# Performance work log

Measured on AMD Instinct MI355X. Metric: run time of the kernel, lower is better.

## Reference

```python
import jax, jax.numpy as jnp
import numpy as np

NUM_HEADS = 16
TOP_K = 6


def setup_inputs() -> dict:
    key = jax.random.key(0)
    ks = jax.random.split(key, 16)
    B, P = 8192, 4096
    QD = PD = D = 1024  # query_dim, prototype_dim, token_dim
    s = lambda d: 1.0 / np.sqrt(d)
    return {
        "query": jax.random.normal(ks[0], (B, QD), jnp.float32),
        "prototype_bank": jax.random.normal(ks[1], (P, PD), jnp.float32),
        "prototype_logits": jax.random.normal(ks[2], (B, P), jnp.float32),
        # query_proj / prototype_proj (torch Linear: y = x @ W.T + b)
        "Wq_proj": jax.random.normal(ks[3], (D, QD), jnp.float32) * s(QD),
        "bq_proj": jnp.zeros((D,), jnp.float32),
        "Wp_proj": jax.random.normal(ks[4], (D, PD), jnp.float32) * s(PD),
        "bp_proj": jnp.zeros((D,), jnp.float32),
        # MultiheadAttention in-proj (q, k, v) and out-proj
        "Wq": jax.random.normal(ks[5], (D, D), jnp.float32) * s(D),
        "bq": jnp.zeros((D,), jnp.float32),
        "Wk": jax.random.normal(ks[6], (D, D), jnp.float32) * s(D),
        "bk": jnp.zeros((D,), jnp.float32),
        "Wv": jax.random.normal(ks[7], (D, D), jnp.float32) * s(D),
        "bv": jnp.zeros((D,), jnp.float32),
        "Wo": jax.random.normal(ks[8], (D, D), jnp.float32) * s(D),
        "bo": jnp.zeros((D,), jnp.float32),
    }


def reference(query, prototype_bank, prototype_logits,
              Wq_proj, bq_proj, Wp_proj, bp_proj,
              Wq, bq, Wk, bk, Wv, bv, Wo, bo):
    B, D = query.shape[0], Wq.shape[0]
    h = NUM_HEADS
    dh = D // h
    k = min(TOP_K, prototype_bank.shape[0])

    # top-k prototype selection (indices only)
    _, topk_idx = jax.lax.top_k(prototype_logits, k)            # [B, k]

    projected_bank = prototype_bank @ Wp_proj.T + bp_proj        # [P, D]
    selected = projected_bank[topk_idx]                          # [B, k, D]

    attn_query = (query @ Wq_proj.T + bq_proj)[:, None, :]       # [B, 1, D]

    # MultiheadAttention (batch_first, eval mode so dropout is a no-op)
    qh = (attn_query @ Wq.T + bq).reshape(B, 1, h, dh).transpose(0, 2, 1, 3)  # [B,h,1,dh]
    kh = (selected @ Wk.T + bk).reshape(B, k, h, dh).transpose(0, 2, 1, 3)    # [B,h,k,dh]
    vh = (selected @ Wv.T + bv).reshape(B, k, h, dh).transpose(0, 2, 1, 3)    # [B,h,k,dh]

    scores = jnp.einsum("bhqd,bhkd->bhqk", qh, kh) / jnp.sqrt(jnp.float32(dh))
    w = jax.nn.softmax(scores, axis=-1)                          # [B,h,1,k]
    ctx = jnp.einsum("bhqk,bhkd->bhqd", w, vh)                   # [B,h,1,dh]
    ctx = ctx.transpose(0, 2, 1, 3).reshape(B, 1, D)
    context = ctx @ Wo.T + bo                                    # [B,1,D]

    attn_weights = w.mean(axis=1)                                # avg heads -> [B,1,k]
    return context[:, 0, :], attn_weights[:, 0, :]
```

## Files before the change

kernel.cpp:

```cpp
#include <hip/hip_runtime.h>
#include <stdint.h>

#define B_ROWS 8192
#define P_ROWS 4096
#define D_DIM  1024
#define K_TOP  6

typedef __attribute__((ext_vector_type(8))) short short8;
typedef __attribute__((ext_vector_type(4))) float floatx4;

static __device__ __forceinline__ float bf2f(unsigned short h) {
  return __uint_as_float(((unsigned)h) << 16);
}
static __device__ __forceinline__ unsigned short f2bf(float f) {
  unsigned u = __float_as_uint(f);
  u += 0x7FFFu + ((u >> 16) & 1u);
  return (unsigned short)(u >> 16);
}

typedef __attribute__((address_space(3))) unsigned int lds32_t;
typedef const __attribute__((address_space(1))) unsigned int g32_t;

static __device__ __forceinline__ void gld_lds16(const unsigned short* g, unsigned short* l) {
  __builtin_amdgcn_global_load_lds((g32_t*)(uintptr_t)g,
                                   (lds32_t*)(unsigned int)(uintptr_t)l, 16, 0, 0);
}

template <bool OUT_BF16, bool HAS_BIAS>
static __device__ __forceinline__ void gemm_bt_body(
    const unsigned short* __restrict__ A, const unsigned short* __restrict__ Bw,
    const float* __restrict__ bias, void* __restrict__ Cout, int m0, int n0) {
  constexpr int Kd = 1024, Nd = 1024, BK = 64;
  __shared__ unsigned short sA[128 * BK];
  __shared__ unsigned short sB[128 * BK];

  const int tid = threadIdx.x;
  const int wid = tid >> 6, lane = tid & 63;
  const int wm = (wid & 1) * 64, wn = (wid >> 1) * 64;

  floatx4 acc[4][4];
#pragma unroll
  for (int mt = 0; mt < 4; ++mt)
#pragma unroll
    for (int nt = 0; nt < 4; ++nt) acc[mt][nt] = (floatx4){0.f, 0.f, 0.f, 0.f};

  const int ld_row = lane >> 3;
  const int ld_col = (lane & 7) * 8;

  for (int kt = 0; kt < Kd / BK; ++kt) {
    const int k0 = kt * BK;
    __syncthreads();
#pragma unroll
    for (int c = 0; c < 4; ++c) {
      const int ch = wid * 4 + c;
      const int r = ch * 8 + ld_row;
      gld_lds16(A  + (size_t)(m0 + r) * Kd + k0 + ld_col, sA + ch * 512);
      gld_lds16(Bw + (size_t)(n0 + r) * Kd + k0 + ld_col, sB + ch * 512);
    }
    __syncthreads();
#pragma unroll
    for (int ks = 0; ks < 2; ++ks) {
      const int kk = ks * 32 + (lane >> 4) * 8;
      short8 a[4], b[4];
#pragma unroll
      for (int t = 0; t < 4; ++t) {
        a[t] = *(const short8*)(sA + (wm + t * 16 + (lane & 15)) * BK + kk);
        b[t] = *(const short8*)(sB + (wn + t * 16 + (lane & 15)) * BK + kk);
      }
#pragma unroll
      for (int mt = 0; mt < 4; ++mt)
#pragma unroll
        for (int nt = 0; nt < 4; ++nt)
          acc[mt][nt] = __builtin_amdgcn_mfma_f32_16x16x32_bf16(a[mt], b[nt], acc[mt][nt], 0, 0, 0);
    }
  }

  const int er = lane >> 4;
  const int ec = lane & 15;
#pragma unroll
  for (int mt = 0; mt < 4; ++mt) {
#pragma unroll
    for (int nt = 0; nt < 4; ++nt) {
      const int col = n0 + wn + nt * 16 + ec;
      const float bv = HAS_BIAS ? bias[col] : 0.f;
#pragma unroll
      for (int r = 0; r < 4; ++r) {
        const int row = m0 + wm + mt * 16 + er * 4 + r;
        const float v = acc[mt][nt][r] + bv;
        if (OUT_BF16)
          ((unsigned short*)Cout)[(size_t)row * Nd + col] = f2bf(v);
        else
          ((float*)Cout)[(size_t)row * Nd + col] = v;
      }
    }
  }
}

template <bool OUT_BF16>
__global__ __launch_bounds__(256) void gemm_bt_kernel(
    const unsigned short* __restrict__ A, const unsigned short* __restrict__ Bw,
    const float* __restrict__ bias, void* __restrict__ Cout) {
  gemm_bt_body<OUT_BF16, true>(A, Bw, bias, Cout, blockIdx.y * 128, blockIdx.x * 128);
}

static __device__ __forceinline__ void cswap64(unsigned long long& hi, unsigned long long& lo) {
  unsigned long long x = hi, y = lo;
  bool c = y > x;
  hi = c ? y : x;
  lo = c ? x : y;
}

static __device__ __forceinline__ unsigned long long topk_key(float val, int idx) {
  unsigned u = __float_as_uint(val);
  u ^= ((unsigned)((int)u >> 31)) | 0x80000000u;
  return (((unsigned long long)u) << 32) | (unsigned long long)(0xFFFFFFFFu - (unsigned)idx);
}

#define PREP_BLOCKS 25856
struct PrepArgs {
  const float* cs[6]; unsigned short* cd[6];
  const float* ts[2]; unsigned short* td[2];
  const float* bW[3]; const float* bp[3]; const float* bb[3]; float* bo[3];
  const float* logits; int* topk;
};

__global__ __launch_bounds__(256) void prep_kernel(PrepArgs a) {
  const int b0 = blockIdx.x;
  if (b0 < 8192) {
    __shared__ float s_tau[4];
    __shared__ int s_cnt;
    __shared__ unsigned long long s_cand[128];
    const int row = b0;
    const int tid = threadIdx.x;
    const int wid = tid >> 6, lane = tid & 63;
    const float4* lp4 = (const float4*)(a.logits + (size_t)row * P_ROWS);

    if (tid == 0) s_cnt = 0;

    float4 r0 = lp4[tid];
    float4 r1 = lp4[256 + tid];
    float4 r2 = lp4[512 + tid];
    float4 r3 = lp4[768 + tid];
    float tmax =
        fmaxf(fmaxf(fmaxf(fmaxf(r0.x, r0.y), fmaxf(r0.z, r0.w)),
                    fmaxf(fmaxf(r1.x, r1.y), fmaxf(r1.z, r1.w))),
              fmaxf(fmaxf(fmaxf(r2.x, r2.y), fmaxf(r2.z, r2.w)),
                    fmaxf(fmaxf(r3.x, r3.y), fmaxf(r3.z, r3.w))));

    float mkeep = tmax, tau = tmax;
#pragma unroll
    for (int it = 0; it < K_TOP; ++it) {
      float best = mkeep;
#pragma unroll
      for (int o = 32; o > 0; o >>= 1) best = fmaxf(best, __shfl_xor(best, o));
      tau = best;
      if (it < K_TOP - 1) mkeep = (mkeep == best) ? -1e38f : mkeep;
    }
    if (lane == 0) s_tau[wid] = tau;
    __syncthreads();
    tau = fmaxf(fmaxf(s_tau[0], s_tau[1]), fmaxf(s_tau[2], s_tau[3]));

    if (tmax >= tau) {
      float4 q0 = lp4[tid];
      float4 q1 = lp4[256 + tid];
      float4 q2 = lp4[512 + tid];
      float4 q3 = lp4[768 + tid];
      auto push = [&](float v, int idx) {
        if (v >= tau) {
          int s = atomicAdd(&s_cnt, 1);
          if (s < 128) s_cand[s] = topk_key(v, idx);
        }
      };
      const int e0 = tid * 4, e1 = 1024 + tid * 4, e2 = 2048 + tid * 4, e3 = 3072 + tid * 4;
      push(q0.x, e0); push(q0.y, e0 + 1); push(q0.z, e0 + 2); push(q0.w, e0 + 3);
      push(q1.x, e1); push(q1.y, e1 + 1); push(q1.z, e1 + 2); push(q1.w, e1 + 3);
      push(q2.x, e2); push(q2.y, e2 + 1); push(q2.z, e2 + 2); push(q2.w, e2 + 3);
      push(q3.x, e3); push(q3.y, e3 + 1); push(q3.z, e3 + 2); push(q3.w, e3 + 3);
    }
    __syncthreads();
    const int n = s_cnt;
    if (wid != 0) return;

    if (n <= 128) {
      unsigned long long k0 = (lane < n) ? s_cand[lane] : 0ull;
      unsigned long long k1 = (lane + 64 < n) ? s_cand[lane + 64] : 0ull;
#pragma unroll
      for (int it = 0; it < K_TOP; ++it) {
        unsigned long long best = k0 > k1 ? k0 : k1;
#pragma unroll
        for (int o = 32; o > 0; o >>= 1) {
          unsigned long long t = __shfl_xor(best, o);
          best = t > best ? t : best;
        }
        if (lane == 0)
          a.topk[row * K_TOP + it] = (int)(0xFFFFFFFFu - (unsigned)(best & 0xFFFFFFFFull));
        k0 = (k0 == best) ? 0ull : k0;
        k1 = (k1 == best) ? 0ull : k1;
      }
    } else {
      unsigned long long m0 = 0, m1 = 0, m2 = 0, m3 = 0, m4 = 0, m5 = 0;
      auto ins = [&](float val, int idx) {
        unsigned long long key = topk_key(val, idx);
        m5 = key > m5 ? key : m5;
        cswap64(m4, m5);
        cswap64(m3, m4);
        cswap64(m2, m3);
        cswap64(m1, m2);
        cswap64(m0, m1);
      };
      for (int j = 0; j < 16; ++j) {
        float4 v = lp4[j * 64 + lane];
        const int base = j * 256 + lane * 4;
        ins(v.x, base);
        ins(v.y, base + 1);
        ins(v.z, base + 2);
        ins(v.w, base + 3);
      }
#pragma unroll
      for (int it = 0; it < K_TOP; ++it) {
        unsigned long long best = m0;
#pragma unroll
        for (int o = 32; o > 0; o >>= 1) {
          unsigned long long t = __shfl_xor(best, o);
          best = t > best ? t : best;
        }
        if (lane == 0)
          a.topk[row * K_TOP + it] = (int)(0xFFFFFFFFu - (unsigned)(best & 0xFFFFFFFFull));
        const bool pred = (m0 == best);
        m0 = pred ? m1 : m0;
        m1 = pred ? m2 : m1;
        m2 = pred ? m3 : m2;
        m3 = pred ? m4 : m3;
        m4 = pred ? m5 : m4;
        m5 = pred ? 0ull : m5;
      }
    }
    return;
  }
  const int b = b0 - 8192;
  if (b < 16384) {
    int seg; unsigned sb;
    if (b < 8192) { seg = 0; sb = 0; }
    else if (b < 12288) { seg = 1; sb = 8192; }
    else { seg = 2 + ((b - 12288) >> 10); sb = 12288u + (((unsigned)(seg - 2)) << 10); }
    const unsigned off = (((unsigned)b - sb) << 10) + threadIdx.x * 4u;
    float4 v = *(const float4*)(a.cs[seg] + off);
    ushort4 o;
    o.x = f2bf(v.x); o.y = f2bf(v.y); o.z = f2bf(v.z); o.w = f2bf(v.w);
    *(ushort4*)(a.cd[seg] + off) = o;
  } else if (b < 16896) {
    __shared__ unsigned short t[64][72];
    const int tt = b - 16384;
    const int which = tt >> 8;
    const int tile = tt & 255;
    const int i0 = (tile >> 4) * 64, j0 = (tile & 15) * 64;
    const float* src = a.ts[which];
    unsigned short* dst = a.td[which];
    const int r = threadIdx.x >> 4;
    const int c = (threadIdx.x & 15) * 4;
#pragma unroll
    for (int rr = 0; rr < 4; ++rr) {
      const int row = r + rr * 16;
      float4 v = *(const float4*)(src + (size_t)(i0 + row) * D_DIM + j0 + c);
      t[c + 0][row] = f2bf(v.x); t[c + 1][row] = f2bf(v.y);
      t[c + 2][row] = f2bf(v.z); t[c + 3][row] = f2bf(v.w);
    }
    __syncthreads();
#pragma unroll
    for (int rr = 0; rr < 4; ++rr) {
      const int row = r + rr * 16;
      ushort4 v = *(const ushort4*)(&t[row][c]);
      *(ushort4*)(dst + (size_t)(j0 + row) * D_DIM + i0 + c) = v;
    }
  } else {
    const int b3 = b - 16896;
    const int j = b3 >> 8;
    const int nb = b3 & 255;
    const int wid = threadIdx.x >> 6, lane = threadIdx.x & 63;
    const int n = nb * 4 + wid;
    const float* W = a.bW[j] + (size_t)n * D_DIM;
    const float* p = a.bp[j];
    float s = 0.f;
#pragma unroll
    for (int d = lane; d < D_DIM; d += 64) s += W[d] * p[d];
#pragma unroll
    for (int o = 32; o > 0; o >>= 1) s += __shfl_xor(s, o);
    if (lane == 0) a.bo[j][n] = s + a.bb[j][n];
  }
}

#define MID_BLOCKS 192
struct MidArgs {
  const unsigned short* fA[3]; const unsigned short* fW[3]; unsigned short* fC[3];
};

__global__ __launch_bounds__(256) void mid_kernel(MidArgs a) {
  const int z = blockIdx.x >> 6;
  const int tile = blockIdx.x & 63;
  gemm_bt_body<true, false>(a.fA[z], a.fW[z], nullptr, (void*)a.fC[z],
                            (tile >> 3) * 128, (tile & 7) * 128);
}

#define GEMM3_BLOCKS 1024
struct Gemm3Args {
  const unsigned short* A[3]; const unsigned short* W[3]; const float* bias[3];
  unsigned short* C[3];
};

__global__ __launch_bounds__(256) void gemm3_kernel(Gemm3Args a) {
  const int b = blockIdx.x;
  int seg, lb;
  if (b < 512) { seg = 0; lb = b; }
  else if (b < 768) { seg = 1; lb = b - 512; }
  else { seg = 2; lb = b - 768; }
  gemm_bt_body<true, true>(a.A[seg], a.W[seg], a.bias[seg], (void*)a.C[seg],
                           (lb >> 3) * 128, (lb & 7) * 128);
}

__global__ __launch_bounds__(256) void attn_kernel(
    const unsigned short* __restrict__ q2,
    const unsigned short* __restrict__ kb,
    const unsigned short* __restrict__ vb,
    const int* __restrict__ topk,
    unsigned short* __restrict__ ctx,
    float* __restrict__ attnw) {
  const int wid = threadIdx.x >> 6, lane = threadIdx.x & 63;
  const int b = blockIdx.x * 4 + wid;

  int idx[K_TOP];
#pragma unroll
  for (int j = 0; j < K_TOP; ++j) idx[j] = topk[b * K_TOP + j];

  const short8* q2r = (const short8*)(q2 + (size_t)b * D_DIM);
  short8 qv0 = q2r[lane], qv1 = q2r[64 + lane];
  float q0[8], q1[8];
#pragma unroll
  for (int i = 0; i < 8; ++i) {
    q0[i] = bf2f((unsigned short)qv0[i]);
    q1[i] = bf2f((unsigned short)qv1[i]);
  }

  float s0[K_TOP], s1[K_TOP];
#pragma unroll
  for (int j = 0; j < K_TOP; ++j) {
    const short8* kr = (const short8*)(kb + (size_t)idx[j] * D_DIM);
    short8 k0 = kr[lane], k1 = kr[64 + lane];
    float p0 = 0.f, p1 = 0.f;
#pragma unroll
    for (int i = 0; i < 8; ++i) {
      p0 += q0[i] * bf2f((unsigned short)k0[i]);
      p1 += q1[i] * bf2f((unsigned short)k1[i]);
    }
    s0[j] = p0; s1[j] = p1;
  }
#pragma unroll
  for (int j = 0; j < K_TOP; ++j) {
#pragma unroll
    for (int o = 1; o < 8; o <<= 1) {
      s0[j] += __shfl_xor(s0[j], o);
      s1[j] += __shfl_xor(s1[j], o);
    }
  }

  float mx0 = -1e30f, mx1 = -1e30f;
#pragma unroll
  for (int j = 0; j < K_TOP; ++j) {
    mx0 = fmaxf(mx0, s0[j] * 0.125f);
    mx1 = fmaxf(mx1, s1[j] * 0.125f);
  }
  float w0[K_TOP], w1[K_TOP], sum0 = 0.f, sum1 = 0.f;
#pragma unroll
  for (int j = 0; j < K_TOP; ++j) {
    w0[j] = __expf(s0[j] * 0.125f - mx0); sum0 += w0[j];
    w1[j] = __expf(s1[j] * 0.125f - mx1); sum1 += w1[j];
  }
  const float inv0 = 1.0f / sum0, inv1 = 1.0f / sum1;
#pragma unroll
  for (int j = 0; j < K_TOP; ++j) { w0[j] *= inv0; w1[j] *= inv1; }

  float o0[8], o1[8];
#pragma unroll
  for (int i = 0; i < 8; ++i) { o0[i] = 0.f; o1[i] = 0.f; }
#pragma unroll
  for (int j = 0; j < K_TOP; ++j) {
    const short8* vr = (const short8*)(vb + (size_t)idx[j] * D_DIM);
    short8 v0 = vr[lane], v1 = vr[64 + lane];
#pragma unroll
    for (int i = 0; i < 8; ++i) {
      o0[i] += w0[j] * bf2f((unsigned short)v0[i]);
      o1[i] += w1[j] * bf2f((unsigned short)v1[i]);
    }
  }
  short8 c0, c1;
#pragma unroll
  for (int i = 0; i < 8; ++i) {
    c0[i] = (short)f2bf(o0[i]);
    c1[i] = (short)f2bf(o1[i]);
  }
  short8* cr = (short8*)(ctx + (size_t)b * D_DIM);
  cr[lane] = c0;
  cr[64 + lane] = c1;

  float t[K_TOP];
#pragma unroll
  for (int j = 0; j < K_TOP; ++j) t[j] = w0[j] + w1[j];
#pragma unroll
  for (int j = 0; j < K_TOP; ++j)
#pragma unroll
    for (int o = 32; o > 0; o >>= 1) t[j] += __shfl_xor(t[j], o);
  if (lane == 0) {
#pragma unroll
    for (int j = 0; j < K_TOP; ++j)
      attnw[(size_t)b * K_TOP + j] = t[j] * (1.0f / 128.0f);
  }
}

extern "C" void kernel_launch(void* const* d_in, const int* in_sizes, int n_in,
                              void* d_out, int out_size, void* d_ws, size_t ws_size,
                              hipStream_t stream) {
  const float* query   = (const float*)d_in[0];
  const float* bank    = (const float*)d_in[1];
  const float* logits  = (const float*)d_in[2];
  const float* Wq_proj = (const float*)d_in[3];
  const float* bq_proj = (const float*)d_in[4];
  const float* Wp_proj = (const float*)d_in[5];
  const float* bp_proj = (const float*)d_in[6];
  const float* Wq      = (const float*)d_in[7];
  const float* bq      = (const float*)d_in[8];
  const float* Wk      = (const float*)d_in[9];
  const float* bk      = (const float*)d_in[10];
  const float* Wv      = (const float*)d_in[11];
  const float* bv      = (const float*)d_in[12];
  const float* Wo      = (const float*)d_in[13];
  const float* bo      = (const float*)d_in[14];

  char* ws = (char*)d_ws;
  size_t off = 0;
  auto alloc = [&](size_t bytes) {
    void* p = ws + off;
    off += (bytes + 255) & ~(size_t)255;
    return p;
  };
  unsigned short* q_bf    = (unsigned short*)alloc((size_t)B_ROWS * D_DIM * 2);
  unsigned short* bank_bf = (unsigned short*)alloc((size_t)P_ROWS * D_DIM * 2);
  unsigned short* q2_bf   = (unsigned short*)alloc((size_t)B_ROWS * D_DIM * 2);
  unsigned short* kb_bf   = (unsigned short*)alloc((size_t)P_ROWS * D_DIM * 2);
  unsigned short* vb_bf   = (unsigned short*)alloc((size_t)P_ROWS * D_DIM * 2);
  unsigned short* wq_bf   = (unsigned short*)alloc((size_t)D_DIM * D_DIM * 2);
  unsigned short* wk_bf   = (unsigned short*)alloc((size_t)D_DIM * D_DIM * 2);
  unsigned short* wv_bf   = (unsigned short*)alloc((size_t)D_DIM * D_DIM * 2);
  unsigned short* wo_bf   = (unsigned short*)alloc((size_t)D_DIM * D_DIM * 2);
  unsigned short* wqpT_bf = (unsigned short*)alloc((size_t)D_DIM * D_DIM * 2);
  unsigned short* wppT_bf = (unsigned short*)alloc((size_t)D_DIM * D_DIM * 2);
  unsigned short* wcq_bf  = (unsigned short*)alloc((size_t)D_DIM * D_DIM * 2);
  unsigned short* wck_bf  = (unsigned short*)alloc((size_t)D_DIM * D_DIM * 2);
  unsigned short* wcv_bf  = (unsigned short*)alloc((size_t)D_DIM * D_DIM * 2);
  float* bcq              = (float*)alloc(D_DIM * 4);
  float* bck              = (float*)alloc(D_DIM * 4);
  float* bcv              = (float*)alloc(D_DIM * 4);
  int* topk               = (int*)alloc((size_t)B_ROWS * K_TOP * 4);

  float* out_ctx  = (float*)d_out;
  float* out_attn = out_ctx + (size_t)B_ROWS * D_DIM;
  (void)out_ctx;

  PrepArgs pa;
  pa.cs[0] = query; pa.cd[0] = q_bf;
  pa.cs[1] = bank;  pa.cd[1] = bank_bf;
  pa.cs[2] = Wq;    pa.cd[2] = wq_bf;
  pa.cs[3] = Wk;    pa.cd[3] = wk_bf;
  pa.cs[4] = Wv;    pa.cd[4] = wv_bf;
  pa.cs[5] = Wo;    pa.cd[5] = wo_bf;
  pa.ts[0] = Wq_proj; pa.td[0] = wqpT_bf;
  pa.ts[1] = Wp_proj; pa.td[1] = wppT_bf;
  pa.bW[0] = Wq; pa.bp[0] = bq_proj; pa.bb[0] = bq; pa.bo[0] = bcq;
  pa.bW[1] = Wk; pa.bp[1] = bp_proj; pa.bb[1] = bk; pa.bo[1] = bck;
  pa.bW[2] = Wv; pa.bp[2] = bp_proj; pa.bb[2] = bv; pa.bo[2] = bcv;
  pa.logits = logits; pa.topk = topk;
  prep_kernel<<<PREP_BLOCKS, 256, 0, stream>>>(pa);

  MidArgs ma;
  ma.fA[0] = wq_bf; ma.fW[0] = wqpT_bf; ma.fC[0] = wcq_bf;
  ma.fA[1] = wk_bf; ma.fW[1] = wppT_bf; ma.fC[1] = wck_bf;
  ma.fA[2] = wv_bf; ma.fW[2] = wppT_bf; ma.fC[2] = wcv_bf;
  mid_kernel<<<MID_BLOCKS, 256, 0, stream>>>(ma);

  Gemm3Args ga;
  ga.A[0] = q_bf;    ga.W[0] = wcq_bf; ga.bias[0] = bcq; ga.C[0] = q2_bf;
  ga.A[1] = bank_bf; ga.W[1] = wck_bf; ga.bias[1] = bck; ga.C[1] = kb_bf;
  ga.A[2] = bank_bf; ga.W[2] = wcv_bf; ga.bias[2] = bcv; ga.C[2] = vb_bf;
  gemm3_kernel<<<GEMM3_BLOCKS, 256, 0, stream>>>(ga);

  attn_kernel<<<B_ROWS / 4, 256, 0, stream>>>(q2_bf, kb_bf, vb_bf, topk, q_bf, out_attn);

  dim3 grid2(D_DIM / 128, B_ROWS / 128);
  gemm_bt_kernel<false><<<grid2, 256, 0, stream>>>(q_bf, wo_bf, bo, d_out);
}
```

Measured before the change: 408.3 us.

## Overlap weight-combine GEMMs with topk and activation casts; swizzle GEMM tile order

Splits the old prep kernel in two. The small weight casts, transposes and bias folding run first. The weight-combine GEMMs (formerly a separate 192-block kernel) then share one launch with the query/bank bf16 casts and per-row top-k, so the tiny GEMM grid no longer leaves the GPU underused. Cast blocks now handle 8 rows each, which cuts block count. The projection and output GEMMs remap block IDs so consecutive blocks walk down M within a column group, aiming for better L2 reuse of the weight tiles.

```diff
diff --git a/kernel.cpp b/kernel.cpp
--- a/kernel.cpp
+++ b/kernel.cpp
@@ -96,13 +96,6 @@
   }
 }
 
-template <bool OUT_BF16>
-__global__ __launch_bounds__(256) void gemm_bt_kernel(
-    const unsigned short* __restrict__ A, const unsigned short* __restrict__ Bw,
-    const float* __restrict__ bias, void* __restrict__ Cout) {
-  gemm_bt_body<OUT_BF16, true>(A, Bw, bias, Cout, blockIdx.y * 128, blockIdx.x * 128);
-}
-
 static __device__ __forceinline__ void cswap64(unsigned long long& hi, unsigned long long& lo) {
   unsigned long long x = hi, y = lo;
   bool c = y > x;
@@ -116,141 +109,29 @@
   return (((unsigned long long)u) << 32) | (unsigned long long)(0xFFFFFFFFu - (unsigned)idx);
 }
 
-#define PREP_BLOCKS 25856
-struct PrepArgs {
-  const float* cs[6]; unsigned short* cd[6];
+#define PREP1_BLOCKS 1792
+struct Prep1Args {
+  const float* ws[4]; unsigned short* wd[4];
   const float* ts[2]; unsigned short* td[2];
   const float* bW[3]; const float* bp[3]; const float* bb[3]; float* bo[3];
-  const float* logits; int* topk;
 };
 
-__global__ __launch_bounds__(256) void prep_kernel(PrepArgs a) {
-  const int b0 = blockIdx.x;
-  if (b0 < 8192) {
-    __shared__ float s_tau[4];
-    __shared__ int s_cnt;
-    __shared__ unsigned long long s_cand[128];
-    const int row = b0;
-    const int tid = threadIdx.x;
-    const int wid = tid >> 6, lane = tid & 63;
-    const float4* lp4 = (const float4*)(a.logits + (size_t)row * P_ROWS);
-
-    if (tid == 0) s_cnt = 0;
-
-    float4 r0 = lp4[tid];
-    float4 r1 = lp4[256 + tid];
-    float4 r2 = lp4[512 + tid];
-    float4 r3 = lp4[768 + tid];
-    float tmax =
-        fmaxf(fmaxf(fmaxf(fmaxf(r0.x, r0.y), fmaxf(r0.z, r0.w)),
-                    fmaxf(fmaxf(r1.x, r1.y), fmaxf(r1.z, r1.w))),
-              fmaxf(fmaxf(fmaxf(r2.x, r2.y), fmaxf(r2.z, r2.w)),
-                    fmaxf(fmaxf(r3.x, r3.y), fmaxf(r3.z, r3.w))));
-
-    float mkeep = tmax, tau = tmax;
-#pragma unroll
-    for (int it = 0; it < K_TOP; ++it) {
-      float best = mkeep;
-#pragma unroll
-      for (int o = 32; o > 0; o >>= 1) best = fmaxf(best, __shfl_xor(best, o));
-      tau = best;
-      if (it < K_TOP - 1) mkeep = (mkeep == best) ? -1e38f : mkeep;
-    }
-    if (lane == 0) s_tau[wid] = tau;
-    __syncthreads();
-    tau = fmaxf(fmaxf(s_tau[0], s_tau[1]), fmaxf(s_tau[2], s_tau[3]));
-
-    if (tmax >= tau) {
-      float4 q0 = lp4[tid];
-      float4 q1 = lp4[256 + tid];
-      float4 q2 = lp4[512 + tid];
-      float4 q3 = lp4[768 + tid];
-      auto push = [&](float v, int idx) {
-        if (v >= tau) {
-          int s = atomicAdd(&s_cnt, 1);
-          if (s < 128) s_cand[s] = topk_key(v, idx);
-        }
-      };
-      const int e0 = tid * 4, e1 = 1024 + tid * 4, e2 = 2048 + tid * 4, e3 = 3072 + tid * 4;
-      push(q0.x, e0); push(q0.y, e0 + 1); push(q0.z, e0 + 2); push(q0.w, e0 + 3);
-      push(q1.x, e1); push(q1.y, e1 + 1); push(q1.z, e1 + 2); push(q1.w, e1 + 3);
-      push(q2.x, e2); push(q2.y, e2 + 1); push(q2.z, e2 + 2); push(q2.w, e2 + 3);
-      push(q3.x, e3); push(q3.y, e3 + 1); push(q3.z, e3 + 2); push(q3.w, e3 + 3);
-    }
-    __syncthreads();
-    const int n = s_cnt;
-    if (wid != 0) return;
-
-    if (n <= 128) {
-      unsigned long long k0 = (lane < n) ? s_cand[lane] : 0ull;
-      unsigned long long k1 = (lane + 64 < n) ? s_cand[lane + 64] : 0ull;
-#pragma unroll
-      for (int it = 0; it < K_TOP; ++it) {
-        unsigned long long best = k0 > k1 ? k0 : k1;
-#pragma unroll
-        for (int o = 32; o > 0; o >>= 1) {
-          unsigned long long t = __shfl_xor(best, o);
-          best = t > best ? t : best;
-        }
-        if (lane == 0)
-          a.topk[row * K_TOP + it] = (int)(0xFFFFFFFFu - (unsigned)(best & 0xFFFFFFFFull));
-        k0 = (k0 == best) ? 0ull : k0;
-        k1 = (k1 == best) ? 0ull : k1;
-      }
-    } else {
-      unsigned long long m0 = 0, m1 = 0, m2 = 0, m3 = 0, m4 = 0, m5 = 0;
-      auto ins = [&](float val, int idx) {
-        unsigned long long key = topk_key(val, idx);
-        m5 = key > m5 ? key : m5;
-        cswap64(m4, m5);
-        cswap64(m3, m4);
-        cswap64(m2, m3);
-        cswap64(m1, m2);
-        cswap64(m0, m1);
-      };
-      for (int j = 0; j < 16; ++j) {
-        float4 v = lp4[j * 64 + lane];
-        const int base = j * 256 + lane * 4;
-        ins(v.x, base);
-        ins(v.y, base + 1);
-        ins(v.z, base + 2);
-        ins(v.w, base + 3);
-      }
-#pragma unroll
-      for (int it = 0; it < K_TOP; ++it) {
-        unsigned long long best = m0;
-#pragma unroll
-        for (int o = 32; o > 0; o >>= 1) {
-          unsigned long long t = __shfl_xor(best, o);
-          best = t > best ? t : best;
-        }
-        if (lane == 0)
-          a.topk[row * K_TOP + it] = (int)(0xFFFFFFFFu - (unsigned)(best & 0xFFFFFFFFull));
-        const bool pred = (m0 == best);
-        m0 = pred ? m1 : m0;
-        m1 = pred ? m2 : m1;
-        m2 = pred ? m3 : m2;
-        m3 = pred ? m4 : m3;
-        m4 = pred ? m5 : m4;
-        m5 = pred ? 0ull : m5;
-      }
-    }
-    return;
-  }
-  const int b = b0 - 8192;
-  if (b < 16384) {
-    int seg; unsigned sb;
-    if (b < 8192) { seg = 0; sb = 0; }
-    else if (b < 12288) { seg = 1; sb = 8192; }
-    else { seg = 2 + ((b - 12288) >> 10); sb = 12288u + (((unsigned)(seg - 2)) << 10); }
-    const unsigned off = (((unsigned)b - sb) << 10) + threadIdx.x * 4u;
-    float4 v = *(const float4*)(a.cs[seg] + off);
-    ushort4 o;
-    o.x = f2bf(v.x); o.y = f2bf(v.y); o.z = f2bf(v.z); o.w = f2bf(v.w);
-    *(ushort4*)(a.cd[seg] + off) = o;
-  } else if (b < 16896) {
+__global__ __launch_bounds__(256) void prep1_kernel(Prep1Args a) {
+  const int b = blockIdx.x;
+  if (b < 512) {
+#pragma unroll
+    for (int u0 = 0; u0 < 8; ++u0) {
+      const int u = b * 8 + u0;
+      const int w = u >> 10;
+      const unsigned off = (((unsigned)u & 1023u) << 10) + threadIdx.x * 4u;
+      float4 v = *(const float4*)(a.ws[w] + off);
+      ushort4 o;
+      o.x = f2bf(v.x); o.y = f2bf(v.y); o.z = f2bf(v.z); o.w = f2bf(v.w);
+      *(ushort4*)(a.wd[w] + off) = o;
+    }
+  } else if (b < 1024) {
     __shared__ unsigned short t[64][72];
-    const int tt = b - 16384;
+    const int tt = b - 512;
     const int which = tt >> 8;
     const int tile = tt & 255;
     const int i0 = (tile >> 4) * 64, j0 = (tile & 15) * 64;
@@ -273,7 +154,7 @@
       *(ushort4*)(dst + (size_t)(j0 + row) * D_DIM + i0 + c) = v;
     }
   } else {
-    const int b3 = b - 16896;
+    const int b3 = b - 1024;
     const int j = b3 >> 8;
     const int nb = b3 & 255;
     const int wid = threadIdx.x >> 6, lane = threadIdx.x & 63;
@@ -289,16 +170,145 @@
   }
 }
 
-#define MID_BLOCKS 192
-struct MidArgs {
+#define FUSED2_BLOCKS 9920
+struct Fused2Args {
   const unsigned short* fA[3]; const unsigned short* fW[3]; unsigned short* fC[3];
+  const float* cs[2]; unsigned short* cd[2];
+  const float* logits; int* topk;
 };
 
-__global__ __launch_bounds__(256) void mid_kernel(MidArgs a) {
-  const int z = blockIdx.x >> 6;
-  const int tile = blockIdx.x & 63;
-  gemm_bt_body<true, false>(a.fA[z], a.fW[z], nullptr, (void*)a.fC[z],
-                            (tile >> 3) * 128, (tile & 7) * 128);
+__global__ __launch_bounds__(256) void fused2_kernel(Fused2Args a) {
+  const int b = blockIdx.x;
+  if (b < 192) {
+    const int z = b >> 6;
+    const int tile = b & 63;
+    gemm_bt_body<true, false>(a.fA[z], a.fW[z], nullptr, (void*)a.fC[z],
+                              (tile >> 3) * 128, (tile & 7) * 128);
+    return;
+  }
+  if (b < 1728) {
+    const int bb = b - 192;
+#pragma unroll
+    for (int u0 = 0; u0 < 8; ++u0) {
+      const int u = bb * 8 + u0;
+      const int seg = (u < 8192) ? 0 : 1;
+      const unsigned local = (seg == 0) ? (unsigned)u : (unsigned)(u - 8192);
+      const unsigned off = (local << 10) + threadIdx.x * 4u;
+      float4 v = *(const float4*)(a.cs[seg] + off);
+      ushort4 o;
+      o.x = f2bf(v.x); o.y = f2bf(v.y); o.z = f2bf(v.z); o.w = f2bf(v.w);
+      *(ushort4*)(a.cd[seg] + off) = o;
+    }
+    return;
+  }
+  __shared__ float s_tau[4];
+  __shared__ int s_cnt;
+  __shared__ unsigned long long s_cand[128];
+  const int row = b - 1728;
+  const int tid = threadIdx.x;
+  const int wid = tid >> 6, lane = tid & 63;
+  const float4* lp4 = (const float4*)(a.logits + (size_t)row * P_ROWS);
+
+  if (tid == 0) s_cnt = 0;
+
+  float4 r0 = lp4[tid];
+  float4 r1 = lp4[256 + tid];
+  float4 r2 = lp4[512 + tid];
+  float4 r3 = lp4[768 + tid];
+  float tmax =
+      fmaxf(fmaxf(fmaxf(fmaxf(r0.x, r0.y), fmaxf(r0.z, r0.w)),
+                  fmaxf(fmaxf(r1.x, r1.y), fmaxf(r1.z, r1.w))),
+            fmaxf(fmaxf(fmaxf(r2.x, r2.y), fmaxf(r2.z, r2.w)),
+                  fmaxf(fmaxf(r3.x, r3.y), fmaxf(r3.z, r3.w))));
+
+  float mkeep = tmax, tau = tmax;
+#pragma unroll
+  for (int it = 0; it < K_TOP; ++it) {
+    float best = mkeep;
+#pragma unroll
+    for (int o = 32; o > 0; o >>= 1) best = fmaxf(best, __shfl_xor(best, o));
+    tau = best;
+    if (it < K_TOP - 1) mkeep = (mkeep == best) ? -1e38f : mkeep;
+  }
+  if (lane == 0) s_tau[wid] = tau;
+  __syncthreads();
+  tau = fmaxf(fmaxf(s_tau[0], s_tau[1]), fmaxf(s_tau[2], s_tau[3]));
+
+  if (tmax >= tau) {
+    float4 q0 = lp4[tid];
+    float4 q1 = lp4[256 + tid];
+    float4 q2 = lp4[512 + tid];
+    float4 q3 = lp4[768 + tid];
+    auto push = [&](float v, int idx) {
+      if (v >= tau) {
+        int s = atomicAdd(&s_cnt, 1);
+        if (s < 128) s_cand[s] = topk_key(v, idx);
+      }
+    };
+    const int e0 = tid * 4, e1 = 1024 + tid * 4, e2 = 2048 + tid * 4, e3 = 3072 + tid * 4;
+    push(q0.x, e0); push(q0.y, e0 + 1); push(q0.z, e0 + 2); push(q0.w, e0 + 3);
+    push(q1.x, e1); push(q1.y, e1 + 1); push(q1.z, e1 + 2); push(q1.w, e1 + 3);
+    push(q2.x, e2); push(q2.y, e2 + 1); push(q2.z, e2 + 2); push(q2.w, e2 + 3);
+    push(q3.x, e3); push(q3.y, e3 + 1); push(q3.z, e3 + 2); push(q3.w, e3 + 3);
+  }
+  __syncthreads();
+  const int n = s_cnt;
+  if (wid != 0) return;
+
+  if (n <= 128) {
+    unsigned long long k0 = (lane < n) ? s_cand[lane] : 0ull;
+    unsigned long long k1 = (lane + 64 < n) ? s_cand[lane + 64] : 0ull;
+#pragma unroll
+    for (int it = 0; it < K_TOP; ++it) {
+      unsigned long long best = k0 > k1 ? k0 : k1;
+#pragma unroll
+      for (int o = 32; o > 0; o >>= 1) {
+        unsigned long long t = __shfl_xor(best, o);
+        best = t > best ? t : best;
+      }
+      if (lane == 0)
+        a.topk[row * K_TOP + it] = (int)(0xFFFFFFFFu - (unsigned)(best & 0xFFFFFFFFull));
+      k0 = (k0 == best) ? 0ull : k0;
+      k1 = (k1 == best) ? 0ull : k1;
+    }
+  } else {
+    unsigned long long m0 = 0, m1 = 0, m2 = 0, m3 = 0, m4 = 0, m5 = 0;
+    auto ins = [&](float val, int idx) {
+      unsigned long long key = topk_key(val, idx);
+      m5 = key > m5 ? key : m5;
+      cswap64(m4, m5);
+      cswap64(m3, m4);
+      cswap64(m2, m3);
+      cswap64(m1, m2);
+      cswap64(m0, m1);
+    };
+    for (int j = 0; j < 16; ++j) {
+      float4 v = lp4[j * 64 + lane];
+      const int base = j * 256 + lane * 4;
+      ins(v.x, base);
+      ins(v.y, base + 1);
+      ins(v.z, base + 2);
+      ins(v.w, base + 3);
+    }
+#pragma unroll
+    for (int it = 0; it < K_TOP; ++it) {
+      unsigned long long best = m0;
+#pragma unroll
+      for (int o = 32; o > 0; o >>= 1) {
+        unsigned long long t = __shfl_xor(best, o);
+        best = t > best ? t : best;
+      }
+      if (lane == 0)
+        a.topk[row * K_TOP + it] = (int)(0xFFFFFFFFu - (unsigned)(best & 0xFFFFFFFFull));
+      const bool pred = (m0 == best);
+      m0 = pred ? m1 : m0;
+      m1 = pred ? m2 : m1;
+      m2 = pred ? m3 : m2;
+      m3 = pred ? m4 : m3;
+      m4 = pred ? m5 : m4;
+      m5 = pred ? 0ull : m5;
+    }
+  }
 }
 
 #define GEMM3_BLOCKS 1024
@@ -309,12 +319,21 @@
 
 __global__ __launch_bounds__(256) void gemm3_kernel(Gemm3Args a) {
   const int b = blockIdx.x;
-  int seg, lb;
-  if (b < 512) { seg = 0; lb = b; }
-  else if (b < 768) { seg = 1; lb = b - 512; }
-  else { seg = 2; lb = b - 768; }
+  int seg, lb, cpx;
+  if (b < 512) { seg = 0; lb = b; cpx = 64; }
+  else if (b < 768) { seg = 1; lb = b - 512; cpx = 32; }
+  else { seg = 2; lb = b - 768; cpx = 32; }
+  const int t = (lb & 7) * cpx + (lb >> 3);
   gemm_bt_body<true, true>(a.A[seg], a.W[seg], a.bias[seg], (void*)a.C[seg],
-                           (lb >> 3) * 128, (lb & 7) * 128);
+                           (t >> 3) * 128, (t & 7) * 128);
+}
+
+__global__ __launch_bounds__(256) void gemm_o_kernel(
+    const unsigned short* __restrict__ A, const unsigned short* __restrict__ Bw,
+    const float* __restrict__ bias, float* __restrict__ Cout) {
+  const int b = blockIdx.x;
+  const int t = (b & 7) * 64 + (b >> 3);
+  gemm_bt_body<false, true>(A, Bw, bias, (void*)Cout, (t >> 3) * 128, (t & 7) * 128);
 }
 
 __global__ __launch_bounds__(256) void attn_kernel(
@@ -462,28 +481,27 @@
 
   float* out_ctx  = (float*)d_out;
   float* out_attn = out_ctx + (size_t)B_ROWS * D_DIM;
-  (void)out_ctx;
-
-  PrepArgs pa;
-  pa.cs[0] = query; pa.cd[0] = q_bf;
-  pa.cs[1] = bank;  pa.cd[1] = bank_bf;
-  pa.cs[2] = Wq;    pa.cd[2] = wq_bf;
-  pa.cs[3] = Wk;    pa.cd[3] = wk_bf;
-  pa.cs[4] = Wv;    pa.cd[4] = wv_bf;
-  pa.cs[5] = Wo;    pa.cd[5] = wo_bf;
+
+  Prep1Args pa;
+  pa.ws[0] = Wq; pa.wd[0] = wq_bf;
+  pa.ws[1] = Wk; pa.wd[1] = wk_bf;
+  pa.ws[2] = Wv; pa.wd[2] = wv_bf;
+  pa.ws[3] = Wo; pa.wd[3] = wo_bf;
   pa.ts[0] = Wq_proj; pa.td[0] = wqpT_bf;
   pa.ts[1] = Wp_proj; pa.td[1] = wppT_bf;
   pa.bW[0] = Wq; pa.bp[0] = bq_proj; pa.bb[0] = bq; pa.bo[0] = bcq;
   pa.bW[1] = Wk; pa.bp[1] = bp_proj; pa.bb[1] = bk; pa.bo[1] = bck;
   pa.bW[2] = Wv; pa.bp[2] = bp_proj; pa.bb[2] = bv; pa.bo[2] = bcv;
-  pa.logits = logits; pa.topk = topk;
-  prep_kernel<<<PREP_BLOCKS, 256, 0, stream>>>(pa);
-
-  MidArgs ma;
-  ma.fA[0] = wq_bf; ma.fW[0] = wqpT_bf; ma.fC[0] = wcq_bf;
-  ma.fA[1] = wk_bf; ma.fW[1] = wppT_bf; ma.fC[1] = wck_bf;
-  ma.fA[2] = wv_bf; ma.fW[2] = wppT_bf; ma.fC[2] = wcv_bf;
-  mid_kernel<<<MID_BLOCKS, 256, 0, stream>>>(ma);
+  prep1_kernel<<<PREP1_BLOCKS, 256, 0, stream>>>(pa);
+
+  Fused2Args fa;
+  fa.fA[0] = wq_bf; fa.fW[0] = wqpT_bf; fa.fC[0] = wcq_bf;
+  fa.fA[1] = wk_bf; fa.fW[1] = wppT_bf; fa.fC[1] = wck_bf;
+  fa.fA[2] = wv_bf; fa.fW[2] = wppT_bf; fa.fC[2] = wcv_bf;
+  fa.cs[0] = query; fa.cd[0] = q_bf;
+  fa.cs[1] = bank;  fa.cd[1] = bank_bf;
+  fa.logits = logits; fa.topk = topk;
+  fused2_kernel<<<FUSED2_BLOCKS, 256, 0, stream>>>(fa);
 
   Gemm3Args ga;
   ga.A[0] = q_bf;    ga.W[0] = wcq_bf; ga.bias[0] = bcq; ga.C[0] = q2_bf;
@@ -493,6 +511,5 @@
 
   attn_kernel<<<B_ROWS / 4, 256, 0, stream>>>(q2_bf, kb_bf, vb_bf, topk, q_bf, out_attn);
 
-  dim3 grid2(D_DIM / 128, B_ROWS / 128);
-  gemm_bt_kernel<false><<<grid2, 256, 0, stream>>>(q_bf, wo_bf, bo, d_out);
-}
+  gemm_o_kernel<<<512, 256, 0, stream>>>(q_bf, wo_bf, bo, (float*)d_out);
+}
```

Measured after the change: 412.1 us. About the same (+1.0%).
